# Optimization experiments

Measured on AMD Instinct MI355X. Metric: run time of the kernel, lower is better.

The kernel has to match this reference:

```python
import jax, jax.numpy as jnp
import numpy as np

HIDDEN = 2048
NUM_HEADS = 8
NUM_KV_HEADS = 2
HEAD_DIM = 256
ROPE_BASE = 1e6
EPS = 1e-6
B, S = 2, 2048


def rms_norm(x, w, eps=EPS):
    # normalize over last dim (head_dim), per-head
    var = jnp.mean(jnp.square(x), axis=-1, keepdims=True)
    return x * jax.lax.rsqrt(var + eps) * w


def rope(x, positions, base=ROPE_BASE):
    # neox-style rotate-half RoPE over full head_dim. x: [B,S,H,D], positions: [B,S]
    d = x.shape[-1]
    inv_freq = 1.0 / (base ** (jnp.arange(0, d, 2, dtype=jnp.float32) / d))
    freqs = positions.astype(jnp.float32)[..., None] * inv_freq  # [B,S,D/2]
    cos = jnp.cos(freqs)[:, :, None, :]
    sin = jnp.sin(freqs)[:, :, None, :]
    x1, x2 = x[..., : d // 2], x[..., d // 2 :]
    return jnp.concatenate([x1 * cos - x2 * sin, x2 * cos + x1 * sin], axis=-1)


def setup_inputs() -> dict:
    key = jax.random.key(0)
    k1, k2, k3 = jax.random.split(key, 3)
    hidden_states = jax.random.normal(k1, (B, S, HIDDEN), dtype=jnp.float32)
    positions = jnp.broadcast_to(jnp.arange(S, dtype=jnp.int32), (B, S))
    qkv_out = (NUM_HEADS + 2 * NUM_KV_HEADS) * HEAD_DIM
    w_qkv = jax.random.normal(k2, (HIDDEN, qkv_out), dtype=jnp.float32) * (HIDDEN ** -0.5)
    w_o = jax.random.normal(k3, (NUM_HEADS * HEAD_DIM, HIDDEN), dtype=jnp.float32) * ((NUM_HEADS * HEAD_DIM) ** -0.5)
    q_norm_w = jnp.ones((HEAD_DIM,), dtype=jnp.float32)
    k_norm_w = jnp.ones((HEAD_DIM,), dtype=jnp.float32)
    return {"hidden_states": hidden_states, "positions": positions, "w_qkv": w_qkv,
            "w_o": w_o, "q_norm_w": q_norm_w, "k_norm_w": k_norm_w}


def reference(hidden_states, positions, w_qkv, w_o, q_norm_w, k_norm_w):
    b, s, _ = hidden_states.shape
    q_size = NUM_HEADS * HEAD_DIM
    kv_size = NUM_KV_HEADS * HEAD_DIM
    qkv = hidden_states @ w_qkv  # [B,S,q+2kv]
    q, k, v = jnp.split(qkv, [q_size, q_size + kv_size], axis=-1)
    q = q.reshape(b, s, NUM_HEADS, HEAD_DIM)
    k = k.reshape(b, s, NUM_KV_HEADS, HEAD_DIM)
    v = v.reshape(b, s, NUM_KV_HEADS, HEAD_DIM)
    # per-head RMSNorm; v_norm has no learned scale (weight fixed to ones)
    q = rms_norm(q, q_norm_w)
    k = rms_norm(k, k_norm_w)
    v = rms_norm(v, jnp.ones((HEAD_DIM,), dtype=v.dtype))
    # RoPE
    q = rope(q, positions)
    k = rope(k, positions)
    # GQA: repeat kv heads
    g = NUM_HEADS // NUM_KV_HEADS
    k = jnp.repeat(k, g, axis=2)
    v = jnp.repeat(v, g, axis=2)
    # causal attention with scaling = 1.0 (as in module)
    scores = jnp.einsum("bqhd,bkhd->bhqk", q, k)
    mask = jnp.tril(jnp.ones((s, s), dtype=bool))
    scores = jnp.where(mask, scores, jnp.finfo(scores.dtype).min)
    probs = jax.nn.softmax(scores, axis=-1)
    attn = jnp.einsum("bhqk,bkhd->bqhd", probs, v).reshape(b, s, NUM_HEADS * HEAD_DIM)
    return attn @ w_o
```

## Files before the change

### kernel.cpp

```cpp
#include <hip/hip_runtime.h>


#define HID  2048
#define NH   8
#define NKV  2
#define HD   256
#define SB   2048
#define BB   2
#define MTOK (BB * SB)
#define NQKV ((NH + 2 * NKV) * HD)

typedef _Float16  f16x8 __attribute__((ext_vector_type(8)));
typedef float     f32x4 __attribute__((ext_vector_type(4)));

__device__ __forceinline__ unsigned short f2h(float f) {
  _Float16 h = (_Float16)f;
  return __builtin_bit_cast(unsigned short, h);
}

__device__ __forceinline__ void async_copy16(const unsigned short* g, unsigned short* l) {
  __builtin_amdgcn_global_load_lds(
      (const __attribute__((address_space(1))) unsigned int*)g,
      (__attribute__((address_space(3))) unsigned int*)l, 16, 0, 0);
}

__device__ __forceinline__ int swz4(int r) { return (r + (r >> 2)) & 3; }

template <int OUT_MODE>
__global__ __launch_bounds__(256) void gemm_bt(const unsigned short* __restrict__ A,
                                               const unsigned short* __restrict__ Bt,
                                               void* __restrict__ Cg,
                                               int M, int N, int K) {
  __shared__ unsigned short Ash[128 * 32];
  __shared__ unsigned short Bsh[128 * 32];
  const int t = threadIdx.x;
  const int lane = t & 63, w = t >> 6;
  const int quad = lane >> 4, m15 = lane & 15;
  const int wm = w >> 1, wn = w & 1;
  const int m0 = blockIdx.y * 128, n0 = blockIdx.x * 128;

  const int rowS0 = t >> 2, rowS1 = rowS0 + 64;
  const int slot = t & 3;
  const int g0 = (slot ^ swz4(rowS0)) * 8;
  const int g1 = (slot ^ swz4(rowS1)) * 8;
  const unsigned short* Ag0 = A + (size_t)(m0 + rowS0) * K + g0;
  const unsigned short* Ag1 = A + (size_t)(m0 + rowS1) * K + g1;
  const unsigned short* Bg0 = Bt + (size_t)(n0 + rowS0) * K + g0;
  const unsigned short* Bg1 = Bt + (size_t)(n0 + rowS1) * K + g1;
  unsigned short* lA0 = &Ash[t * 8];
  unsigned short* lA1 = &Ash[(t + 256) * 8];
  unsigned short* lB0 = &Bsh[t * 8];
  unsigned short* lB1 = &Bsh[(t + 256) * 8];

  int offA[4], offB[4];
#pragma unroll
  for (int i = 0; i < 4; ++i) {
    const int ra = wm * 64 + i * 16 + m15;
    offA[i] = ra * 32 + (quad ^ swz4(ra)) * 8;
    const int rb = wn * 64 + i * 16 + m15;
    offB[i] = rb * 32 + (quad ^ swz4(rb)) * 8;
  }

  const f32x4 vz = {0.f, 0.f, 0.f, 0.f};
  f32x4 acc[4][4];
#pragma unroll
  for (int i = 0; i < 4; ++i)
#pragma unroll
    for (int j = 0; j < 4; ++j) acc[i][j] = vz;

  const int nk = K >> 5;
  for (int kt = 0; kt < nk; ++kt) {
    const int k0 = kt * 32;
    async_copy16(Ag0 + k0, lA0);
    async_copy16(Ag1 + k0, lA1);
    async_copy16(Bg0 + k0, lB0);
    async_copy16(Bg1 + k0, lB1);
    __syncthreads();
    f16x8 af[4], bfr[4];
#pragma unroll
    for (int i = 0; i < 4; ++i) af[i] = *(const f16x8*)&Ash[offA[i]];
#pragma unroll
    for (int j = 0; j < 4; ++j) bfr[j] = *(const f16x8*)&Bsh[offB[j]];
#pragma unroll
    for (int i = 0; i < 4; ++i)
#pragma unroll
      for (int j = 0; j < 4; ++j)
        acc[i][j] = __builtin_amdgcn_mfma_f32_16x16x32_f16(af[i], bfr[j], acc[i][j], 0, 0, 0);
    __syncthreads();
  }

#pragma unroll
  for (int i = 0; i < 4; ++i)
#pragma unroll
    for (int j = 0; j < 4; ++j)
#pragma unroll
      for (int r = 0; r < 4; ++r) {
        const int gm = m0 + wm * 64 + i * 16 + quad * 4 + r;
        const int gn = n0 + wn * 64 + j * 16 + m15;
        const float v = acc[i][j][r];
        if (OUT_MODE == 2) ((float*)Cg)[(size_t)gm * N + gn] = v;
        else               ((unsigned short*)Cg)[(size_t)gm * N + gn] = f2h(v);
      }
}

__global__ __launch_bounds__(256) void cvt_f32_f16(const float* __restrict__ in,
                                                   unsigned short* __restrict__ out, int n4) {
  const int i = blockIdx.x * 256 + threadIdx.x;
  if (i >= n4) return;
  const float4 v = ((const float4*)in)[i];
  ushort4 o = {f2h(v.x), f2h(v.y), f2h(v.z), f2h(v.w)};
  ((ushort4*)out)[i] = o;
}

__global__ __launch_bounds__(256) void transpose_f2h(const float* __restrict__ in,
                                                     unsigned short* __restrict__ out,
                                                     int R, int C) {
  __shared__ float tile[64 * 68];
  const int r0 = blockIdx.y * 64, c0 = blockIdx.x * 64;
  const int t = threadIdx.x;
#pragma unroll
  for (int p = 0; p < 4; ++p) {
    const int idx = t + p * 256;
    const int rr = idx >> 4, cc = (idx & 15) * 4;
    *(float4*)&tile[rr * 68 + cc] = *(const float4*)&in[(size_t)(r0 + rr) * C + c0 + cc];
  }
  __syncthreads();
#pragma unroll
  for (int p = 0; p < 2; ++p) {
    const int idx = t + p * 256;
    const int dr = idx >> 3, sc = (idx & 7) * 8;
    union { uint4 v; unsigned short s[8]; } o;
#pragma unroll
    for (int e = 0; e < 8; ++e) o.s[e] = f2h(tile[(sc + e) * 68 + dr]);
    *(uint4*)&out[(size_t)(c0 + dr) * R + r0 + sc] = o.v;
  }
}

__global__ __launch_bounds__(256) void normrope(const unsigned short* __restrict__ qkv,
                                                const int* __restrict__ pos,
                                                const float* __restrict__ qw,
                                                const float* __restrict__ kw,
                                                unsigned short* __restrict__ Qh,
                                                unsigned short* __restrict__ Kh,
                                                unsigned short* __restrict__ Vh) {
  const int tok = blockIdx.x;
  const int b = tok >> 11, s = tok & 2047;
  const int t = threadIdx.x, w = t >> 6, lane = t & 63;
  const float p = (float)pos[tok];
  const int dbase = lane * 4;

  for (int it = 0; it < 3; ++it) {
    const int slot = it * 4 + w;
    const unsigned short* src = qkv + (size_t)tok * NQKV + slot * 256 + dbase;
    union { uint2 u; _Float16 h[4]; } rd;
    rd.u = *(const uint2*)src;
    float y[4];
#pragma unroll
    for (int e = 0; e < 4; ++e) y[e] = (float)rd.h[e];
    float ssq = y[0] * y[0] + y[1] * y[1] + y[2] * y[2] + y[3] * y[3];
#pragma unroll
    for (int off = 1; off < 64; off <<= 1) ssq += __shfl_xor(ssq, off);
    const float rn = rsqrtf(ssq * (1.f / 256.f) + 1e-6f);

    if (slot < 8) {
#pragma unroll
      for (int e = 0; e < 4; ++e) y[e] *= rn * qw[dbase + e];
    } else if (slot < 10) {
#pragma unroll
      for (int e = 0; e < 4; ++e) y[e] *= rn * kw[dbase + e];
    } else {
#pragma unroll
      for (int e = 0; e < 4; ++e) y[e] *= rn;
    }

    unsigned short* dst;
    if (slot < 8)       dst = Qh + ((size_t)(b * NH + slot) * SB + s) * HD + dbase;
    else if (slot < 10) dst = Kh + ((size_t)(b * NKV + slot - 8) * SB + s) * HD + dbase;
    else                dst = Vh + ((size_t)(b * NKV + slot - 10) * SB + s) * HD + dbase;

    float outv[4];
    if (slot < 10) {
      const int i0 = dbase & 127;
      const bool lo = (lane < 32);
#pragma unroll
      for (int e = 0; e < 4; ++e) {
        const float partner = __shfl_xor(y[e], 32);
        const float invf = expf(-(float)(i0 + e) * 0.10793368f);
        const float fr = p * invf;
        const float cv = cosf(fr), sv = sinf(fr);
        outv[e] = lo ? (y[e] * cv - partner * sv) : (y[e] * cv + partner * sv);
      }
    } else {
#pragma unroll
      for (int e = 0; e < 4; ++e) outv[e] = y[e];
    }
    union { uint2 u; _Float16 h[4]; } wr;
#pragma unroll
    for (int e = 0; e < 4; ++e) wr.h[e] = (_Float16)outv[e];
    *(uint2*)dst = wr.u;
  }
}

__global__ __launch_bounds__(256) void transpose_u16(const unsigned short* __restrict__ in,
                                                     unsigned short* __restrict__ out,
                                                     int R, int C, size_t ibs, size_t obs) {
  __shared__ unsigned short tile[64 * 72];
  const unsigned short* ib = in + blockIdx.z * ibs;
  unsigned short* ob = out + blockIdx.z * obs;
  const int r0 = blockIdx.y * 64, c0 = blockIdx.x * 64;
  const int t = threadIdx.x;
#pragma unroll
  for (int pck = 0; pck < 2; ++pck) {
    const int c = t + pck * 256;
    const int rr = c >> 3, cc = (c & 7) * 8;
    *(uint4*)&tile[rr * 72 + cc] = *(const uint4*)&ib[(size_t)(r0 + rr) * C + c0 + cc];
  }
  __syncthreads();
#pragma unroll
  for (int pck = 0; pck < 2; ++pck) {
    const int c = t + pck * 256;
    const int dr = c >> 3, sc = (c & 7) * 8;
    union { uint4 v; unsigned short s[8]; } o;
#pragma unroll
    for (int e = 0; e < 8; ++e) o.s[e] = tile[(sc + e) * 72 + dr];
    *(uint4*)&ob[(size_t)(c0 + dr) * R + r0 + sc] = o.v;
  }
}

__global__ __launch_bounds__(512, 2) void flash_attn(const unsigned short* __restrict__ Qh,
                                                     const unsigned short* __restrict__ Kh,
                                                     const unsigned short* __restrict__ Vt,
                                                     unsigned short* __restrict__ attn) {
  __shared__ unsigned short Ksh[2][64 * 256];
  __shared__ unsigned short Vsh[2][256 * 64];
  __shared__ _Float16 Psh[8][16 * 72];
  const int pairi = blockIdx.x;
  const int h = blockIdx.y, b = blockIdx.z;
  const int kv = h >> 2;
  const int t = threadIdx.x, w = t >> 6, lane = t & 63;
  const int wq = w & 3, team = w >> 2;
  const int quad = lane >> 4, m15 = lane & 15;

  const unsigned short* Kb = Kh + (size_t)(b * NKV + kv) * SB * HD;
  const unsigned short* Vb = Vt + (size_t)(b * NKV + kv) * HD * SB;

  const int krow = t >> 5, kchunk = t & 31;
  const int vrow = t >> 3, vchunk = t & 7;

  const int pshx = ((m15 >> 2) & 3) << 3;

  const f32x4 vz = {0.f, 0.f, 0.f, 0.f};

  for (int jb = 0; jb < 2; ++jb) {
    const int qt = jb ? (31 - pairi) : pairi;
    const int q0 = qt * 64, qw0 = q0 + wq * 16;

    f16x8 aq[8];
    const unsigned short* qb = Qh + ((size_t)(b * NH + h) * SB + qw0 + m15) * HD + quad * 8;
#pragma unroll
    for (int ks = 0; ks < 8; ++ks) aq[ks] = *(const f16x8*)(qb + ks * 32);

    f32x4 o[8];
#pragma unroll
    for (int i = 0; i < 8; ++i) o[i] = vz;
    float mrow[4] = {-1e30f, -1e30f, -1e30f, -1e30f};
    float lrow[4] = {0.f, 0.f, 0.f, 0.f};

    const int nkt = (q0 + 64) >> 6;

#pragma unroll
    for (int shot = 0; shot < 4; ++shot) {
      const int r = krow + 16 * shot;
      async_copy16(Kb + (size_t)r * HD + ((kchunk ^ (r & 7)) * 8),
                   &Ksh[0][4096 * shot + t * 8]);
    }
#pragma unroll
    for (int shot = 0; shot < 4; ++shot) {
      const int d = vrow + 64 * shot;
      async_copy16(Vb + (size_t)d * SB + ((vchunk ^ (d & 7)) * 8),
                   &Vsh[0][4096 * shot + t * 8]);
    }
    __syncthreads();

    for (int kt = 0; kt < nkt; ++kt) {
      const int k0 = kt * 64;
      const int par = kt & 1;

      if (kt + 1 < nkt) {
        const int kn = k0 + 64;
        const int pn = par ^ 1;
#pragma unroll
        for (int shot = 0; shot < 4; ++shot) {
          const int r = krow + 16 * shot;
          async_copy16(Kb + (size_t)(kn + r) * HD + ((kchunk ^ (r & 7)) * 8),
                       &Ksh[pn][4096 * shot + t * 8]);
        }
#pragma unroll
        for (int shot = 0; shot < 4; ++shot) {
          const int d = vrow + 64 * shot;
          async_copy16(Vb + (size_t)d * SB + kn + ((vchunk ^ (d & 7)) * 8),
                       &Vsh[pn][4096 * shot + t * 8]);
        }
      }

      const unsigned short* KB = &Ksh[par][0];
      const unsigned short* VB = &Vsh[par][0];

      f32x4 sv[4];
#pragma unroll
      for (int g = 0; g < 4; ++g) sv[g] = vz;
#pragma unroll
      for (int g = 0; g < 4; ++g) {
        const int key = g * 16 + m15;
        const unsigned short* kr = &KB[key * 256];
        const int sw = (key & 7);
#pragma unroll
        for (int ks = 0; ks < 8; ++ks) {
          const f16x8 bk = *(const f16x8*)&kr[((4 * ks + quad) ^ sw) * 8];
          sv[g] = __builtin_amdgcn_mfma_f32_16x16x32_f16(aq[ks], bk, sv[g], 0, 0, 0);
        }
      }

      const bool last = (kt == nkt - 1);
#pragma unroll
      for (int r = 0; r < 4; ++r) {
        const int q = qw0 + quad * 4 + r;
        float s[4];
#pragma unroll
        for (int g = 0; g < 4; ++g) {
          s[g] = sv[g][r];
          if (last && (k0 + g * 16 + m15) > q) s[g] = -3.0e38f;
        }
        float tm = fmaxf(fmaxf(s[0], s[1]), fmaxf(s[2], s[3]));
#pragma unroll
        for (int off = 1; off < 16; off <<= 1) tm = fmaxf(tm, __shfl_xor(tm, off));
        const float mnew = fmaxf(mrow[r], tm);
        const float alpha = __expf(mrow[r] - mnew);
        float p[4], rs = 0.f;
#pragma unroll
        for (int g = 0; g < 4; ++g) { p[g] = __expf(s[g] - mnew); rs += p[g]; }
#pragma unroll
        for (int off = 1; off < 16; off <<= 1) rs += __shfl_xor(rs, off);
        lrow[r] = lrow[r] * alpha + rs;
        mrow[r] = mnew;
#pragma unroll
        for (int dbi = 0; dbi < 8; ++dbi) o[dbi][r] *= alpha;
        _Float16* pr = &Psh[w][(quad * 4 + r) * 72];
        const int wx = quad << 3;
#pragma unroll
        for (int g = 0; g < 4; ++g) pr[(g * 16 + m15) ^ wx] = (_Float16)p[g];
      }

      asm volatile("" ::: "memory");
#pragma unroll
      for (int c = 0; c < 2; ++c) {
        const f16x8 ap = *(const f16x8*)&Psh[w][m15 * 72 + ((c * 32 + quad * 8) ^ pshx)];
#pragma unroll
        for (int i = 0; i < 8; ++i) {
          const int d = (team * 8 + i) * 16 + m15;
          const f16x8 bv = *(const f16x8*)&VB[d * 64 + (((4 * c + quad) ^ (d & 7)) * 8)];
          o[i] = __builtin_amdgcn_mfma_f32_16x16x32_f16(ap, bv, o[i], 0, 0, 0);
        }
      }

      __syncthreads();
    }

    float inv[4];
#pragma unroll
    for (int r = 0; r < 4; ++r) inv[r] = 1.0f / lrow[r];
#pragma unroll
    for (int i = 0; i < 8; ++i)
#pragma unroll
      for (int r = 0; r < 4; ++r) {
        const int q = qw0 + quad * 4 + r;
        const int col = h * HD + (team * 8 + i) * 16 + m15;
        attn[(size_t)(b * SB + q) * (NH * HD) + col] = f2h(o[i][r] * inv[r]);
      }
  }
}

static constexpr size_t OFF_HB   = 0;
static constexpr size_t OFF_QH   = 0;
static constexpr size_t OFF_W1T  = 16777216;
static constexpr size_t OFF_KH   = 16777216;
static constexpr size_t OFF_VH   = 20971520;
static constexpr size_t OFF_VT   = 25165824;
static constexpr size_t OFF_WOT  = 29360128;
static constexpr size_t OFF_QKV  = 37748736;
static constexpr size_t OFF_ATTN = OFF_QKV;

extern "C" void kernel_launch(void* const* d_in, const int* in_sizes, int n_in,
                              void* d_out, int out_size, void* d_ws, size_t ws_size,
                              hipStream_t stream) {
  const float* hidden    = (const float*)d_in[0];
  const int*   positions = (const int*)d_in[1];
  const float* w_qkv     = (const float*)d_in[2];
  const float* w_o       = (const float*)d_in[3];
  const float* qw        = (const float*)d_in[4];
  const float* kw        = (const float*)d_in[5];
  float* out = (float*)d_out;
  char* ws = (char*)d_ws;

  unsigned short* hb    = (unsigned short*)(ws + OFF_HB);
  unsigned short* wqkvT = (unsigned short*)(ws + OFF_W1T);
  unsigned short* woT   = (unsigned short*)(ws + OFF_WOT);
  unsigned short* qkvb  = (unsigned short*)(ws + OFF_QKV);
  unsigned short* attnb = (unsigned short*)(ws + OFF_ATTN);
  unsigned short* Qhb   = (unsigned short*)(ws + OFF_QH);
  unsigned short* Khb   = (unsigned short*)(ws + OFF_KH);
  unsigned short* Vhb   = (unsigned short*)(ws + OFF_VH);
  unsigned short* Vtb   = (unsigned short*)(ws + OFF_VT);

  cvt_f32_f16<<<dim3((MTOK * HID / 4 + 255) / 256), 256, 0, stream>>>(hidden, hb, MTOK * HID / 4);
  transpose_f2h<<<dim3(NQKV / 64, HID / 64), 256, 0, stream>>>(w_qkv, wqkvT, HID, NQKV);
  transpose_f2h<<<dim3(HID / 64, HID / 64), 256, 0, stream>>>(w_o, woT, HID, HID);

  gemm_bt<0><<<dim3(NQKV / 128, MTOK / 128), 256, 0, stream>>>(hb, wqkvT, qkvb, MTOK, NQKV, HID);

  normrope<<<dim3(MTOK), 256, 0, stream>>>(qkvb, positions, qw, kw, Qhb, Khb, Vhb);

  transpose_u16<<<dim3(HD / 64, SB / 64, BB * NKV), 256, 0, stream>>>(Vhb, Vtb, SB, HD,
                                                                     (size_t)SB * HD, (size_t)SB * HD);

  flash_attn<<<dim3(16, NH, BB), 512, 0, stream>>>(Qhb, Khb, Vtb, attnb);

  gemm_bt<2><<<dim3(HID / 128, MTOK / 128), 256, 0, stream>>>(attnb, woT, out, MTOK, HID, HID);
}
```

Measured before the change: 385.6 us.

## Split flash attention keys across wave teams and merge partial softmax states

Result: faster. 362.4 us (-6.0%).

```diff
diff --git a/kernel.cpp b/kernel.cpp
--- a/kernel.cpp
+++ b/kernel.cpp
@@ -231,9 +231,13 @@
                                                      const unsigned short* __restrict__ Kh,
                                                      const unsigned short* __restrict__ Vt,
                                                      unsigned short* __restrict__ attn) {
-  __shared__ unsigned short Ksh[2][64 * 256];
-  __shared__ unsigned short Vsh[2][256 * 64];
-  __shared__ _Float16 Psh[8][16 * 72];
+  __shared__ __align__(16) unsigned char SMEM[142336];
+  unsigned short* Ksh = (unsigned short*)SMEM;
+  unsigned short* Vsh = (unsigned short*)(SMEM + 65536);
+  _Float16*      Psh  = (_Float16*)(SMEM + 131072);
+  float*         MLx  = (float*)(SMEM + 141312);
+  float*         mergeO = (float*)SMEM;
+
   const int pairi = blockIdx.x;
   const int h = blockIdx.y, b = blockIdx.z;
   const int kv = h >> 2;
@@ -247,8 +251,6 @@
   const int krow = t >> 5, kchunk = t & 31;
   const int vrow = t >> 3, vchunk = t & 7;
 
-  const int pshx = ((m15 >> 2) & 3) << 3;
-
   const f32x4 vz = {0.f, 0.f, 0.f, 0.f};
 
   for (int jb = 0; jb < 2; ++jb) {
@@ -260,9 +262,9 @@
 #pragma unroll
     for (int ks = 0; ks < 8; ++ks) aq[ks] = *(const f16x8*)(qb + ks * 32);
 
-    f32x4 o[8];
-#pragma unroll
-    for (int i = 0; i < 8; ++i) o[i] = vz;
+    f32x4 o[16];
+#pragma unroll
+    for (int i = 0; i < 16; ++i) o[i] = vz;
     float mrow[4] = {-1e30f, -1e30f, -1e30f, -1e30f};
     float lrow[4] = {0.f, 0.f, 0.f, 0.f};
 
@@ -272,13 +274,13 @@
     for (int shot = 0; shot < 4; ++shot) {
       const int r = krow + 16 * shot;
       async_copy16(Kb + (size_t)r * HD + ((kchunk ^ (r & 7)) * 8),
-                   &Ksh[0][4096 * shot + t * 8]);
+                   &Ksh[4096 * shot + t * 8]);
     }
 #pragma unroll
     for (int shot = 0; shot < 4; ++shot) {
       const int d = vrow + 64 * shot;
       async_copy16(Vb + (size_t)d * SB + ((vchunk ^ (d & 7)) * 8),
-                   &Vsh[0][4096 * shot + t * 8]);
+                   &Vsh[4096 * shot + t * 8]);
     }
     __syncthreads();
 
@@ -293,25 +295,24 @@
         for (int shot = 0; shot < 4; ++shot) {
           const int r = krow + 16 * shot;
           async_copy16(Kb + (size_t)(kn + r) * HD + ((kchunk ^ (r & 7)) * 8),
-                       &Ksh[pn][4096 * shot + t * 8]);
+                       &Ksh[pn * 16384 + 4096 * shot + t * 8]);
         }
 #pragma unroll
         for (int shot = 0; shot < 4; ++shot) {
           const int d = vrow + 64 * shot;
           async_copy16(Vb + (size_t)d * SB + kn + ((vchunk ^ (d & 7)) * 8),
-                       &Vsh[pn][4096 * shot + t * 8]);
-        }
-      }
-
-      const unsigned short* KB = &Ksh[par][0];
-      const unsigned short* VB = &Vsh[par][0];
-
-      f32x4 sv[4];
-#pragma unroll
-      for (int g = 0; g < 4; ++g) sv[g] = vz;
-#pragma unroll
-      for (int g = 0; g < 4; ++g) {
-        const int key = g * 16 + m15;
+                       &Vsh[pn * 16384 + 4096 * shot + t * 8]);
+        }
+      }
+
+      const unsigned short* KB = &Ksh[par * 16384];
+      const unsigned short* VB = &Vsh[par * 16384];
+
+      f32x4 sv[2];
+      sv[0] = vz; sv[1] = vz;
+#pragma unroll
+      for (int g = 0; g < 2; ++g) {
+        const int key = team * 32 + g * 16 + m15;
         const unsigned short* kr = &KB[key * 256];
         const int sw = (key & 7);
 #pragma unroll
@@ -325,58 +326,89 @@
 #pragma unroll
       for (int r = 0; r < 4; ++r) {
         const int q = qw0 + quad * 4 + r;
-        float s[4];
-#pragma unroll
-        for (int g = 0; g < 4; ++g) {
+        float s[2];
+#pragma unroll
+        for (int g = 0; g < 2; ++g) {
           s[g] = sv[g][r];
-          if (last && (k0 + g * 16 + m15) > q) s[g] = -3.0e38f;
-        }
-        float tm = fmaxf(fmaxf(s[0], s[1]), fmaxf(s[2], s[3]));
+          if (last && (k0 + team * 32 + g * 16 + m15) > q) s[g] = -3.0e38f;
+        }
+        float tm = fmaxf(s[0], s[1]);
 #pragma unroll
         for (int off = 1; off < 16; off <<= 1) tm = fmaxf(tm, __shfl_xor(tm, off));
         const float mnew = fmaxf(mrow[r], tm);
         const float alpha = __expf(mrow[r] - mnew);
-        float p[4], rs = 0.f;
-#pragma unroll
-        for (int g = 0; g < 4; ++g) { p[g] = __expf(s[g] - mnew); rs += p[g]; }
+        float p[2], rs;
+        p[0] = __expf(s[0] - mnew);
+        p[1] = __expf(s[1] - mnew);
+        rs = p[0] + p[1];
 #pragma unroll
         for (int off = 1; off < 16; off <<= 1) rs += __shfl_xor(rs, off);
         lrow[r] = lrow[r] * alpha + rs;
         mrow[r] = mnew;
 #pragma unroll
-        for (int dbi = 0; dbi < 8; ++dbi) o[dbi][r] *= alpha;
-        _Float16* pr = &Psh[w][(quad * 4 + r) * 72];
+        for (int dbi = 0; dbi < 16; ++dbi) o[dbi][r] *= alpha;
+        _Float16* pr = &Psh[w * 640 + (quad * 4 + r) * 40];
         const int wx = quad << 3;
-#pragma unroll
-        for (int g = 0; g < 4; ++g) pr[(g * 16 + m15) ^ wx] = (_Float16)p[g];
+        pr[(m15) ^ wx]      = (_Float16)p[0];
+        pr[(16 + m15) ^ wx] = (_Float16)p[1];
       }
 
       asm volatile("" ::: "memory");
-#pragma unroll
-      for (int c = 0; c < 2; ++c) {
-        const f16x8 ap = *(const f16x8*)&Psh[w][m15 * 72 + ((c * 32 + quad * 8) ^ pshx)];
-#pragma unroll
-        for (int i = 0; i < 8; ++i) {
-          const int d = (team * 8 + i) * 16 + m15;
-          const f16x8 bv = *(const f16x8*)&VB[d * 64 + (((4 * c + quad) ^ (d & 7)) * 8)];
-          o[i] = __builtin_amdgcn_mfma_f32_16x16x32_f16(ap, bv, o[i], 0, 0, 0);
+      {
+        const f16x8 ap = *(const f16x8*)&Psh[w * 640 + m15 * 40 + ((quad ^ (m15 >> 2)) << 3)];
+#pragma unroll
+        for (int dbi = 0; dbi < 16; ++dbi) {
+          const int d = dbi * 16 + m15;
+          const f16x8 bv = *(const f16x8*)&VB[d * 64 + (((team * 4 + quad) ^ (d & 7)) * 8)];
+          o[dbi] = __builtin_amdgcn_mfma_f32_16x16x32_f16(ap, bv, o[dbi], 0, 0, 0);
         }
       }
 
       __syncthreads();
     }
 
-    float inv[4];
-#pragma unroll
-    for (int r = 0; r < 4; ++r) inv[r] = 1.0f / lrow[r];
-#pragma unroll
-    for (int i = 0; i < 8; ++i)
+    if (m15 == 0) {
 #pragma unroll
       for (int r = 0; r < 4; ++r) {
-        const int q = qw0 + quad * 4 + r;
-        const int col = h * HD + (team * 8 + i) * 16 + m15;
-        attn[(size_t)(b * SB + q) * (NH * HD) + col] = f2h(o[i][r] * inv[r]);
-      }
+        MLx[w * 32 + (quad * 4 + r) * 2]     = mrow[r];
+        MLx[w * 32 + (quad * 4 + r) * 2 + 1] = lrow[r];
+      }
+    }
+    {
+      float* mo = mergeO + w * 2080;
+#pragma unroll
+      for (int ii = 0; ii < 8; ++ii) {
+        const int i = team ? ii : (8 + ii);
+        const int dcol = ii * 16 + m15;
+#pragma unroll
+        for (int r = 0; r < 4; ++r) mo[(quad * 4 + r) * 130 + dcol] = o[i][r];
+      }
+    }
+    __syncthreads();
+    {
+      const int pw = w ^ 4;
+      const float* pmo = mergeO + pw * 2080;
+#pragma unroll
+      for (int r = 0; r < 4; ++r) {
+        const int row = quad * 4 + r;
+        const int q = qw0 + row;
+        const float pm = MLx[pw * 32 + row * 2];
+        const float pl = MLx[pw * 32 + row * 2 + 1];
+        const float m = fmaxf(mrow[r], pm);
+        const float a0 = __expf(mrow[r] - m);
+        const float a1 = __expf(pm - m);
+        const float invl = 1.0f / (a0 * lrow[r] + a1 * pl);
+#pragma unroll
+        for (int ii = 0; ii < 8; ++ii) {
+          const int i = team ? (8 + ii) : ii;
+          const float po = pmo[row * 130 + ii * 16 + m15];
+          const float val = (a0 * o[i][r] + a1 * po) * invl;
+          const int col = h * HD + team * 128 + ii * 16 + m15;
+          attn[(size_t)(b * SB + q) * (NH * HD) + col] = f2h(val);
+        }
+      }
+    }
+    __syncthreads();
   }
 }
 
```
